# Kernel optimization log

Measured on AMD Instinct MI355X. Metric: run time of the kernel, lower is better.

Reference implementation:

```python
import jax, jax.numpy as jnp
import numpy as np
import math

B, C, H, W = 16, 512, 32, 32
GROUPS = 32
EPS = 1e-5


def group_norm(x, w, b):
    # x: [B, C, H, W]; normalize within each of GROUPS channel groups over (C//G, H, W)
    Bx, Cx, Hx, Wx = x.shape
    xg = x.reshape(Bx, GROUPS, Cx // GROUPS, Hx, Wx)
    mean = xg.mean(axis=(2, 3, 4), keepdims=True)
    var = xg.var(axis=(2, 3, 4), keepdims=True)
    xg = (xg - mean) * jax.lax.rsqrt(var + EPS)
    xn = xg.reshape(Bx, Cx, Hx, Wx)
    return xn * w[None, :, None, None] + b[None, :, None, None]


def setup_inputs() -> dict:
    key = jax.random.key(0)
    ks = jax.random.split(key, 4)
    x = jax.random.normal(ks[0], (B, C, H, W), dtype=jnp.float32)
    gn_w = jnp.ones((C,), dtype=jnp.float32)
    gn_b = jnp.zeros((C,), dtype=jnp.float32)
    # Conv2d 1x1 weights as [out, in] matrices; PyTorch default init scale
    qkv_w = jax.random.normal(ks[1], (3 * C, C), dtype=jnp.float32) * (1.0 / math.sqrt(C))
    qkv_b = jnp.zeros((3 * C,), dtype=jnp.float32)
    out_w = jax.random.normal(ks[2], (C, C), dtype=jnp.float32) * (1.0 / math.sqrt(C))
    out_b = jnp.zeros((C,), dtype=jnp.float32)
    return {"x": x, "gn_w": gn_w, "gn_b": gn_b, "qkv_w": qkv_w,
            "qkv_b": qkv_b, "out_w": out_w, "out_b": out_b}


def reference(x, gn_w, gn_b, qkv_w, qkv_b, out_w, out_b):
    Bx, Cx, Hx, Wx = x.shape
    N = Hx * Wx
    h = group_norm(x, gn_w, gn_b)                       # [B, C, H, W]
    hf = h.reshape(Bx, Cx, N)                           # [B, C, N]
    # 1x1 conv == channel matmul
    qkv = jnp.einsum('oc,bcn->bon', qkv_w, hf) + qkv_b[None, :, None]  # [B, 3C, N]
    q, k, v = jnp.split(qkv, 3, axis=1)                 # each [B, C, N]
    q = q.transpose(0, 2, 1)                            # [B, N, C]
    v = v.transpose(0, 2, 1)                            # [B, N, C]
    scale = 1.0 / math.sqrt(Cx)
    attn = jnp.einsum('bnc,bcm->bnm', q, k) * scale     # [B, N, N]
    attn = jax.nn.softmax(attn, axis=-1)
    o = jnp.einsum('bnm,bmc->bnc', attn, v)             # [B, N, C]
    o = o.transpose(0, 2, 1)                            # [B, C, N]
    o = jnp.einsum('oc,bcn->bon', out_w, o) + out_b[None, :, None]
    return x + o.reshape(Bx, Cx, Hx, Wx)
```

## Files before the change

kernel.cpp:

```cpp
#include <hip/hip_runtime.h>

typedef unsigned short u16;
typedef short short8 __attribute__((ext_vector_type(8)));
typedef float floatx4 __attribute__((ext_vector_type(4)));
typedef u16 u16x4 __attribute__((ext_vector_type(4)));
typedef u16 u16x8 __attribute__((ext_vector_type(8)));

#define DEVI __device__ __forceinline__

DEVI u16 f2bf(float x) {
    union { float f; unsigned u; } c; c.f = x;
    unsigned u = c.u;
    u += 0x7fffu + ((u >> 16) & 1u);
    return (u16)(u >> 16);
}
DEVI u16 f2bf_fast(float x) {
    union { float f; unsigned u; } c; c.f = x;
    return (u16)((c.u + 0x8000u) >> 16);
}
DEVI float bf2f(u16 h) {
    union { unsigned u; float f; } c; c.u = ((unsigned)h) << 16;
    return c.f;
}

DEVI void gload_lds16(const void* g, void* l) {
    auto gp = (const __attribute__((address_space(1))) unsigned*)(unsigned long long)g;
    auto lp = (__attribute__((address_space(3))) unsigned*)(unsigned)(unsigned long long)l;
    __builtin_amdgcn_global_load_lds(gp, lp, 16, 0, 0);
}

__global__ __launch_bounds__(256) void gn_fused_kernel(const float* __restrict__ x,
                                                       const float* __restrict__ w,
                                                       const float* __restrict__ bb,
                                                       u16* __restrict__ h) {
    const int bg = blockIdx.x;
    const int b = bg >> 5, g = bg & 31;
    const float* xg = x + (long long)bg * 16384;
    const int n0 = threadIdx.x * 4;

    float4 xv[16];
    float s = 0.f, s2 = 0.f;
    #pragma unroll
    for (int cc = 0; cc < 16; cc++) {
        xv[cc] = *(const float4*)&xg[cc * 1024 + n0];
        s  += xv[cc].x + xv[cc].y + xv[cc].z + xv[cc].w;
        s2 += xv[cc].x*xv[cc].x + xv[cc].y*xv[cc].y + xv[cc].z*xv[cc].z + xv[cc].w*xv[cc].w;
    }
    #pragma unroll
    for (int m = 1; m < 64; m <<= 1) { s += __shfl_xor(s, m, 64); s2 += __shfl_xor(s2, m, 64); }
    __shared__ float rs[4], rq[4];
    if ((threadIdx.x & 63) == 0) { rs[threadIdx.x >> 6] = s; rq[threadIdx.x >> 6] = s2; }
    __syncthreads();
    float mean = (rs[0] + rs[1] + rs[2] + rs[3]) * (1.f / 16384.f);
    float var  = (rq[0] + rq[1] + rq[2] + rq[3]) * (1.f / 16384.f) - mean * mean;
    float rstd = rsqrtf(var + 1e-5f);

    u16x8 o[4][2];
    #pragma unroll
    for (int cc = 0; cc < 16; cc++) {
        int c = g * 16 + cc;
        float sc = w[c] * rstd;
        float sh = bb[c] - mean * sc;
        o[0][cc >> 3][cc & 7] = f2bf(xv[cc].x * sc + sh);
        o[1][cc >> 3][cc & 7] = f2bf(xv[cc].y * sc + sh);
        o[2][cc >> 3][cc & 7] = f2bf(xv[cc].z * sc + sh);
        o[3][cc >> 3][cc & 7] = f2bf(xv[cc].w * sc + sh);
    }
    u16* hb = h + ((long long)b * 1024 + n0) * 512 + g * 16;
    #pragma unroll
    for (int k = 0; k < 4; k++) {
        *(u16x8*)&hb[(long long)k * 512]     = o[k][0];
        *(u16x8*)&hb[(long long)k * 512 + 8] = o[k][1];
    }
}

__global__ __launch_bounds__(256) void wconv_kernel(const float* __restrict__ w1, u16* __restrict__ o1,
                                                    const float* __restrict__ w2, u16* __restrict__ o2) {
    int i = blockIdx.x * 256 + threadIdx.x;
    const float* src; u16* dst; int j;
    if (i < 196608) { src = w1; dst = o1; j = i; }
    else            { src = w2; dst = o2; j = i - 196608; }
    float4 v = *(const float4*)&src[j * 4];
    u16x4 p; p[0] = f2bf(v.x); p[1] = f2bf(v.y); p[2] = f2bf(v.z); p[3] = f2bf(v.w);
    *(u16x4*)&dst[j * 4] = p;
}

__global__ __launch_bounds__(256) void lreduce_kernel(const float* __restrict__ ps,
                                                      float* __restrict__ invl) {
    int i = blockIdx.x * 256 + threadIdx.x;
    int z = i >> 10, n = i & 1023;
    float l = 0.f;
    #pragma unroll
    for (int kb = 0; kb < 8; kb++) l += ps[((z * 8 + kb) << 10) + n];
    invl[i] = 1.f / l;
}

template <int MODE, int NX, int NY, bool STATS>
__global__ __launch_bounds__(256, 3)
void gemm_bt_kernel(const u16* __restrict__ A, const u16* __restrict__ Bt,
                    void* __restrict__ C0,
                    const float* __restrict__ bias, const float* __restrict__ res,
                    float* __restrict__ aux,
                    float scale, int lda, int ldb, int ldc,
                    long long sA, long long sB, long long sC, long long sR, int K) {
    int bx, by, bz;
    if (NX > 0) {
        const int lid  = blockIdx.x;
        const int xcd  = lid & 7;
        const int slot = lid >> 3;
        const int per  = NX * NY;
        const int j    = slot / per;
        const int w    = slot - j * per;
        bz = xcd + 8 * j;
        bx = w % NX;
        by = w / NX;
    } else {
        bx = blockIdx.x; by = blockIdx.y; bz = blockIdx.z;
    }
    const int t    = threadIdx.x;
    const int lane = t & 63;
    const int wave = t >> 6;
    const int m0   = by * 128;
    const int n0   = bx * 128;
    A  += (long long)bz * sA;
    Bt += (long long)bz * sB;

    __shared__ __align__(16) u16 smem[16384];
    u16* As = smem;
    u16* Bs = smem + 8192;

    const int wm = wave >> 1, wn = wave & 1;
    const int quad = lane >> 4, lrow = lane & 15;

    floatx4 acc[4][4];
    #pragma unroll
    for (int i = 0; i < 4; i++)
        #pragma unroll
        for (int j = 0; j < 4; j++)
            #pragma unroll
            for (int r = 0; r < 4; r++) acc[i][j][r] = 0.f;

    const int rowA = t >> 2;
    const int kch  = (t & 3) * 8;
    const u16* Ag = A  + (long long)(m0 + rowA) * lda + kch;
    const u16* Bg = Bt + (long long)(n0 + rowA) * ldb + kch;
    u16* Al = &As[t * 8];
    u16* Bl = &Bs[t * 8];
    const long long a64 = (long long)64 * lda;
    const long long b64 = (long long)64 * ldb;
    const u16* Bg3 = Bt + (long long)n0 * ldb;

    for (int k0 = 0; k0 < K; k0 += 64) {
        gload_lds16(Ag + k0,            Al);
        gload_lds16(Ag + k0 + a64,      Al + 2048);
        gload_lds16(Ag + k0 + 32,       Al + 4096);
        gload_lds16(Ag + k0 + 32 + a64, Al + 6144);
        if (MODE != 3) {
            gload_lds16(Bg + k0,            Bl);
            gload_lds16(Bg + k0 + b64,      Bl + 2048);
            gload_lds16(Bg + k0 + 32,       Bl + 4096);
            gload_lds16(Bg + k0 + 32 + b64, Bl + 6144);
        } else {
            #pragma unroll
            for (int q = 0; q < 4; q++) {
                const int row = ((q & 1) ? 64 : 0) + (t >> 2);
                const int kc  = (q >> 1) * 32 + (t & 3) * 8;
                u16x8 sv = *(const u16x8*)&Bg3[(long long)row * ldb + k0 + kc];
                u16x8 ev;
                #pragma unroll
                for (int e = 0; e < 8; e++)
                    ev[e] = f2bf_fast(__expf(bf2f(sv[e])));
                *(u16x8*)&Bs[q * 2048 + t * 8] = ev;
            }
        }
        __syncthreads();
        #pragma unroll
        for (int kk = 0; kk < 2; kk++) {
            short8 af[4], bfr[4];
            #pragma unroll
            for (int i = 0; i < 4; i++)
                af[i] = *(const short8*)&As[kk*4096 + (wm*64 + i*16 + lrow)*32 + quad*8];
            #pragma unroll
            for (int j = 0; j < 4; j++)
                bfr[j] = *(const short8*)&Bs[kk*4096 + (wn*64 + j*16 + lrow)*32 + quad*8];
            #pragma unroll
            for (int i = 0; i < 4; i++)
                #pragma unroll
                for (int j = 0; j < 4; j++)
                    acc[i][j] = __builtin_amdgcn_mfma_f32_16x16x32_bf16(af[i], bfr[j], acc[i][j], 0, 0, 0);
        }
        __syncthreads();
    }

    const int ST = 136;

    if (MODE == 1) {
        #pragma unroll
        for (int p = 0; p < 4; p++) {
            if (p) __syncthreads();
            if (wm == (p >> 1)) {
                #pragma unroll
                for (int ii = 0; ii < 2; ii++) {
                    const int i = (p & 1) * 2 + ii;
                    const int row = ii * 16 + quad * 4;
                    #pragma unroll
                    for (int j = 0; j < 4; j++) {
                        const int cB = wn * 64 + j * 16 + lrow;
                        #pragma unroll
                        for (int r = 0; r < 4; r++)
                            smem[(row + r) * ST + cB] = f2bf(acc[i][j][r] * scale);
                    }
                }
            }
            __syncthreads();
            const int rr = t >> 3, cc = (t & 7) * 16;
            u16x8 a0 = *(u16x8*)&smem[rr * ST + cc];
            u16x8 a1 = *(u16x8*)&smem[rr * ST + cc + 8];
            u16* Cp = (u16*)C0 + (long long)bz * sC + (long long)(m0 + p * 32 + rr) * ldc + n0 + cc;
            *(u16x8*)Cp = a0;
            *(u16x8*)(Cp + 8) = a1;
            if (STATS) {
                float ls = 0.f;
                #pragma unroll
                for (int e = 0; e < 8; e++)
                    ls += __expf(bf2f(a0[e])) + __expf(bf2f(a1[e]));
                #pragma unroll
                for (int m2 = 1; m2 < 8; m2 <<= 1) ls += __shfl_xor(ls, m2, 8);
                if ((t & 7) == 0)
                    aux[((long long)(bz * 8 + bx)) * 1024 + m0 + p * 32 + rr] = ls;
            }
        }
    } else if (MODE == 2) {
        #pragma unroll
        for (int p = 0; p < 4; p++) {
            if (p) __syncthreads();
            if (wn == (p >> 1)) {
                #pragma unroll
                for (int jj = 0; jj < 2; jj++) {
                    const int j = (p & 1) * 2 + jj;
                    const int row = jj * 16 + lrow;
                    #pragma unroll
                    for (int i = 0; i < 4; i++) {
                        const int mmL = wm * 64 + i * 16 + quad * 4;
                        u16x4 pk;
                        #pragma unroll
                        for (int r = 0; r < 4; r++)
                            pk[r] = f2bf(acc[i][j][r] + bias[m0 + mmL + r]);
                        *(u16x4*)&smem[row * ST + mmL] = pk;
                    }
                }
            }
            __syncthreads();
            const int rr = t >> 3, cc = (t & 7) * 16;
            u16x8 a0 = *(u16x8*)&smem[rr * ST + cc];
            u16x8 a1 = *(u16x8*)&smem[rr * ST + cc + 8];
            u16* Cp = (u16*)C0 + (long long)(n0 + p * 32 + rr) * ldc + m0 + cc;
            *(u16x8*)Cp = a0;
            *(u16x8*)(Cp + 8) = a1;
        }
    } else {
        float* smf = (float*)smem;
        const int SF = 132;
        float* C = (float*)C0 + (long long)bz * sC;
        const float* rz = res + (long long)bz * sR;
        const float* il = aux + (long long)bz * 1024;
        #pragma unroll
        for (int p = 0; p < 8; p++) {
            if (p) __syncthreads();
            if (wm == (p >> 2)) {
                const int i = p & 3;
                #pragma unroll
                for (int j = 0; j < 4; j++) {
                    const int cB = wn * 64 + j * 16 + lrow;
                    #pragma unroll
                    for (int r = 0; r < 4; r++)
                        smf[(quad * 4 + r) * SF + cB] = acc[i][j][r];
                }
            }
            __syncthreads();
            const int rr = t >> 4, cc = (t & 15) * 8;
            const float bsv = bias[m0 + p * 16 + rr];
            float4 il0 = *(const float4*)&il[n0 + cc];
            float4 il1 = *(const float4*)&il[n0 + cc + 4];
            const long long gro = (long long)(m0 + p * 16 + rr) * ldc + n0 + cc;
            float4 rv0 = *(const float4*)&rz[gro];
            float4 rv1 = *(const float4*)&rz[gro + 4];
            float4 ov0, ov1;
            ov0.x = smf[rr*SF + cc + 0] * il0.x + bsv + rv0.x;
            ov0.y = smf[rr*SF + cc + 1] * il0.y + bsv + rv0.y;
            ov0.z = smf[rr*SF + cc + 2] * il0.z + bsv + rv0.z;
            ov0.w = smf[rr*SF + cc + 3] * il0.w + bsv + rv0.w;
            ov1.x = smf[rr*SF + cc + 4] * il1.x + bsv + rv1.x;
            ov1.y = smf[rr*SF + cc + 5] * il1.y + bsv + rv1.y;
            ov1.z = smf[rr*SF + cc + 6] * il1.z + bsv + rv1.z;
            ov1.w = smf[rr*SF + cc + 7] * il1.w + bsv + rv1.w;
            *(float4*)&C[gro]     = ov0;
            *(float4*)&C[gro + 4] = ov1;
        }
    }
}

extern "C" void kernel_launch(void* const* d_in, const int* in_sizes, int n_in,
                              void* d_out, int out_size, void* d_ws, size_t ws_size,
                              hipStream_t stream) {
    (void)in_sizes; (void)n_in; (void)out_size; (void)ws_size;
    const float* x     = (const float*)d_in[0];
    const float* gn_w  = (const float*)d_in[1];
    const float* gn_b  = (const float*)d_in[2];
    const float* qkv_w = (const float*)d_in[3];
    const float* qkv_b = (const float*)d_in[4];
    const float* out_w = (const float*)d_in[5];
    const float* out_b = (const float*)d_in[6];
    float* out = (float*)d_out;

    char* ws = (char*)d_ws;
    u16*  h_t   = (u16*)ws;  ws += (size_t)16*1024*512*2;
    u16*  qkv_t = (u16*)ws;  ws += (size_t)16*1024*1536*2;
    u16*  vprm  = (u16*)ws;  ws += (size_t)512*16384*2;
    u16*  S     = (u16*)ws;  ws += (size_t)16*1024*1024*2;
    u16*  wq    = (u16*)ws;  ws += (size_t)1536*512*2;
    u16*  wo    = (u16*)ws;  ws += (size_t)512*512*2;
    float* psum = (float*)ws; ws += (size_t)16*8*1024*4;
    float* invl = (float*)ws; ws += (size_t)16*1024*4;

    wconv_kernel<<<1024, 256, 0, stream>>>(qkv_w, wq, out_w, wo);
    gn_fused_kernel<<<512, 256, 0, stream>>>(x, gn_w, gn_b, h_t);

    gemm_bt_kernel<2, 0, 0, false><<<dim3(128, 12, 1), 256, 0, stream>>>(
        wq, h_t, qkv_t, qkv_b, nullptr, nullptr, 1.0f,
        512, 512, 1536, 0, 0, 0, 0, 512);

    gemm_bt_kernel<1, 0, 0, false><<<dim3(128, 4, 1), 256, 0, stream>>>(
        wo, qkv_t + 1024, vprm, nullptr, nullptr, nullptr, 1.0f,
        512, 1536, 16384, 0, 0, 0, 0, 512);

    gemm_bt_kernel<1, 8, 8, true><<<1024, 256, 0, stream>>>(
        qkv_t, qkv_t + 512, S, nullptr, nullptr, psum, 0.044194173824159216f,
        1536, 1536, 1024,
        (long long)1024*1536, (long long)1024*1536, (long long)1024*1024, 0, 512);

    lreduce_kernel<<<64, 256, 0, stream>>>(psum, invl);

    gemm_bt_kernel<3, 8, 4, false><<<512, 256, 0, stream>>>(
        vprm, S, out, out_b, x, invl, 1.0f,
        16384, 1024, 1024,
        1024, (long long)1024*1024, (long long)512*1024, (long long)512*1024, 1024);
}
```

Before: 213.6 us.

## Use dedicated 64x64-tile kernel for QK^T scores and fold row-sum reduction into output GEMM

Replaces the 128x128-tile QK^T score GEMM with a new 64x64-tile kernel launched as 4096 blocks at higher occupancy. It still writes bf16 scores and per-tile exp row-sums. The separate lreduce kernel is removed: the final PV/out-projection GEMM now sums the 16 partial sums per column itself and stores the reciprocals in shared memory. This drops one launch and one global round trip and spreads the score GEMM over more blocks. The cost is smaller tiles with less reuse and redundant partial-sum reads in every output block.

```diff
diff --git a/kernel.cpp b/kernel.cpp
--- a/kernel.cpp
+++ b/kernel.cpp
@@ -85,22 +85,98 @@
     *(u16x4*)&dst[j * 4] = p;
 }
 
-__global__ __launch_bounds__(256) void lreduce_kernel(const float* __restrict__ ps,
-                                                      float* __restrict__ invl) {
-    int i = blockIdx.x * 256 + threadIdx.x;
-    int z = i >> 10, n = i & 1023;
-    float l = 0.f;
-    #pragma unroll
-    for (int kb = 0; kb < 8; kb++) l += ps[((z * 8 + kb) << 10) + n];
-    invl[i] = 1.f / l;
-}
-
-template <int MODE, int NX, int NY, bool STATS>
+__global__ __launch_bounds__(256, 6)
+void gemm_s64_kernel(const u16* __restrict__ A, const u16* __restrict__ Bt,
+                     u16* __restrict__ C, float* __restrict__ psum,
+                     float scale, int lda, long long sAB, long long sC, int K) {
+    const int lid  = blockIdx.x;
+    const int xcd  = lid & 7;
+    const int slot = lid >> 3;
+    const int j    = slot >> 8;
+    const int w    = slot & 255;
+    const int bz   = xcd + 8 * j;
+    const int bx   = w & 15, by = w >> 4;
+    const int m0   = by * 64, n0 = bx * 64;
+    A  += (long long)bz * sAB;
+    Bt += (long long)bz * sAB;
+
+    __shared__ __align__(16) u16 smem[8192];
+    u16* As = smem;
+    u16* Bs = smem + 4096;
+
+    const int t = threadIdx.x, lane = t & 63, wave = t >> 6;
+    const int wm = wave >> 1, wn = wave & 1;
+    const int quad = lane >> 4, lrow = lane & 15;
+
+    floatx4 acc[2][2];
+    #pragma unroll
+    for (int i = 0; i < 2; i++)
+        #pragma unroll
+        for (int jj = 0; jj < 2; jj++)
+            #pragma unroll
+            for (int r = 0; r < 4; r++) acc[i][jj][r] = 0.f;
+
+    const u16* Ag = A  + (long long)(m0 + (t >> 2)) * lda + (t & 3) * 8;
+    const u16* Bg = Bt + (long long)(n0 + (t >> 2)) * lda + (t & 3) * 8;
+    u16* Al = &As[t * 8];
+    u16* Bl = &Bs[t * 8];
+
+    for (int k0 = 0; k0 < K; k0 += 64) {
+        gload_lds16(Ag + k0,      Al);
+        gload_lds16(Ag + k0 + 32, Al + 2048);
+        gload_lds16(Bg + k0,      Bl);
+        gload_lds16(Bg + k0 + 32, Bl + 2048);
+        __syncthreads();
+        #pragma unroll
+        for (int kk = 0; kk < 2; kk++) {
+            short8 af[2], bfr[2];
+            #pragma unroll
+            for (int i = 0; i < 2; i++)
+                af[i] = *(const short8*)&As[kk*2048 + (wm*32 + i*16 + lrow)*32 + quad*8];
+            #pragma unroll
+            for (int jj = 0; jj < 2; jj++)
+                bfr[jj] = *(const short8*)&Bs[kk*2048 + (wn*32 + jj*16 + lrow)*32 + quad*8];
+            #pragma unroll
+            for (int i = 0; i < 2; i++)
+                #pragma unroll
+                for (int jj = 0; jj < 2; jj++)
+                    acc[i][jj] = __builtin_amdgcn_mfma_f32_16x16x32_bf16(af[i], bfr[jj], acc[i][jj], 0, 0, 0);
+        }
+        __syncthreads();
+    }
+
+    const int ST = 72;
+    #pragma unroll
+    for (int i = 0; i < 2; i++)
+        #pragma unroll
+        for (int jj = 0; jj < 2; jj++)
+            #pragma unroll
+            for (int r = 0; r < 4; r++)
+                smem[(wm*32 + i*16 + quad*4 + r)*ST + wn*32 + jj*16 + lrow] =
+                    f2bf(acc[i][jj][r] * scale);
+    __syncthreads();
+    const int rr = t >> 2, cc = (t & 3) * 16;
+    u16x8 a0 = *(u16x8*)&smem[rr * ST + cc];
+    u16x8 a1 = *(u16x8*)&smem[rr * ST + cc + 8];
+    u16* Cp = C + (long long)bz * sC + (long long)(m0 + rr) * 1024 + n0 + cc;
+    *(u16x8*)Cp = a0;
+    *(u16x8*)(Cp + 8) = a1;
+    float ls = 0.f;
+    #pragma unroll
+    for (int e = 0; e < 8; e++)
+        ls += __expf(bf2f(a0[e])) + __expf(bf2f(a1[e]));
+    ls += __shfl_xor(ls, 1, 4);
+    ls += __shfl_xor(ls, 2, 4);
+    if ((t & 3) == 0)
+        psum[(((long long)bz * 16 + bx) << 10) + m0 + rr] = ls;
+}
+
+template <int MODE, int NX, int NY>
 __global__ __launch_bounds__(256, 3)
 void gemm_bt_kernel(const u16* __restrict__ A, const u16* __restrict__ Bt,
                     void* __restrict__ C0,
                     const float* __restrict__ bias, const float* __restrict__ res,
-                    float* __restrict__ aux,
+                    const float* __restrict__ aux,
                     float scale, int lda, int ldb, int ldc,
                     long long sA, long long sB, long long sC, long long sR, int K) {
     int bx, by, bz;
@@ -219,16 +295,6 @@
             u16* Cp = (u16*)C0 + (long long)bz * sC + (long long)(m0 + p * 32 + rr) * ldc + n0 + cc;
             *(u16x8*)Cp = a0;
             *(u16x8*)(Cp + 8) = a1;
-            if (STATS) {
-                float ls = 0.f;
-                #pragma unroll
-                for (int e = 0; e < 8; e++)
-                    ls += __expf(bf2f(a0[e])) + __expf(bf2f(a1[e]));
-                #pragma unroll
-                for (int m2 = 1; m2 < 8; m2 <<= 1) ls += __shfl_xor(ls, m2, 8);
-                if ((t & 7) == 0)
-                    aux[((long long)(bz * 8 + bx)) * 1024 + m0 + p * 32 + rr] = ls;
-            }
         }
     } else if (MODE == 2) {
         #pragma unroll
@@ -261,9 +327,9 @@
     } else {
         float* smf = (float*)smem;
         const int SF = 132;
+        float* invsh = smf + 2176;
         float* C = (float*)C0 + (long long)bz * sC;
         const float* rz = res + (long long)bz * sR;
-        const float* il = aux + (long long)bz * 1024;
         #pragma unroll
         for (int p = 0; p < 8; p++) {
             if (p) __syncthreads();
@@ -277,11 +343,18 @@
                         smf[(quad * 4 + r) * SF + cB] = acc[i][j][r];
                 }
             }
+            if (p == 0 && t < 128) {
+                float l = 0.f;
+                #pragma unroll
+                for (int kb = 0; kb < 16; kb++)
+                    l += aux[(((long long)bz * 16 + kb) << 10) + n0 + t];
+                invsh[t] = 1.f / l;
+            }
             __syncthreads();
             const int rr = t >> 4, cc = (t & 15) * 8;
             const float bsv = bias[m0 + p * 16 + rr];
-            float4 il0 = *(const float4*)&il[n0 + cc];
-            float4 il1 = *(const float4*)&il[n0 + cc + 4];
+            float4 il0 = *(const float4*)&invsh[cc];
+            float4 il1 = *(const float4*)&invsh[cc + 4];
             const long long gro = (long long)(m0 + p * 16 + rr) * ldc + n0 + cc;
             float4 rv0 = *(const float4*)&rz[gro];
             float4 rv1 = *(const float4*)&rz[gro + 4];
@@ -320,29 +393,25 @@
     u16*  S     = (u16*)ws;  ws += (size_t)16*1024*1024*2;
     u16*  wq    = (u16*)ws;  ws += (size_t)1536*512*2;
     u16*  wo    = (u16*)ws;  ws += (size_t)512*512*2;
-    float* psum = (float*)ws; ws += (size_t)16*8*1024*4;
-    float* invl = (float*)ws; ws += (size_t)16*1024*4;
+    float* psum = (float*)ws; ws += (size_t)16*16*1024*4;
 
     wconv_kernel<<<1024, 256, 0, stream>>>(qkv_w, wq, out_w, wo);
     gn_fused_kernel<<<512, 256, 0, stream>>>(x, gn_w, gn_b, h_t);
 
-    gemm_bt_kernel<2, 0, 0, false><<<dim3(128, 12, 1), 256, 0, stream>>>(
+    gemm_bt_kernel<2, 0, 0><<<dim3(128, 12, 1), 256, 0, stream>>>(
         wq, h_t, qkv_t, qkv_b, nullptr, nullptr, 1.0f,
         512, 512, 1536, 0, 0, 0, 0, 512);
 
-    gemm_bt_kernel<1, 0, 0, false><<<dim3(128, 4, 1), 256, 0, stream>>>(
+    gemm_bt_kernel<1, 0, 0><<<dim3(128, 4, 1), 256, 0, stream>>>(
         wo, qkv_t + 1024, vprm, nullptr, nullptr, nullptr, 1.0f,
         512, 1536, 16384, 0, 0, 0, 0, 512);
 
-    gemm_bt_kernel<1, 8, 8, true><<<1024, 256, 0, stream>>>(
-        qkv_t, qkv_t + 512, S, nullptr, nullptr, psum, 0.044194173824159216f,
-        1536, 1536, 1024,
-        (long long)1024*1536, (long long)1024*1536, (long long)1024*1024, 0, 512);
-
-    lreduce_kernel<<<64, 256, 0, stream>>>(psum, invl);
-
-    gemm_bt_kernel<3, 8, 4, false><<<512, 256, 0, stream>>>(
-        vprm, S, out, out_b, x, invl, 1.0f,
+    gemm_s64_kernel<<<4096, 256, 0, stream>>>(
+        qkv_t, qkv_t + 512, S, psum, 0.044194173824159216f,
+        1536, (long long)1024*1536, (long long)1024*1024, 512);
+
+    gemm_bt_kernel<3, 8, 4><<<512, 256, 0, stream>>>(
+        vprm, S, out, out_b, x, psum, 1.0f,
         16384, 1024, 1024,
         1024, (long long)1024*1024, (long long)512*1024, (long long)512*1024, 1024);
 }
```

Measured after the change: 222.4 us. 4.2% more time.
